# Optimization experiments

Measured on AMD Instinct MI355X. Metric: run time of the kernel, lower is better.

The kernel has to match this reference:

```python
import jax, jax.numpy as jnp
import numpy as np

SEQ_LEN = 70      # hardcoded in original (view(-1, 70))
HIDDEN = 230
EMB = 50
VOCAB = 100000
BIG_NUM = 64
N_TOTAL = 2048
N_REL = 100       # hardcoded relation count
POS_VOCAB = 123
POS_DIM = 5
D_IN = EMB + 2 * POS_DIM


def setup_inputs() -> dict:
    key = jax.random.key(0)
    ks = jax.random.split(key, 20)
    bag = N_TOTAL // BIG_NUM
    labels = jax.random.randint(ks[3], (BIG_NUM,), 0, N_REL)
    inp = {
        "sentence": jax.random.randint(ks[0], (N_TOTAL, SEQ_LEN), 0, VOCAB),
        "pos1": jax.random.randint(ks[1], (N_TOTAL, SEQ_LEN), 0, POS_VOCAB),
        "pos2": jax.random.randint(ks[2], (N_TOTAL, SEQ_LEN), 0, POS_VOCAB),
        "total_shape": jnp.arange(BIG_NUM + 1, dtype=jnp.int32) * bag,
        "y_batch": jax.nn.one_hot(labels, N_REL, dtype=jnp.float32),
        "word_emb": jax.random.normal(ks[4], (VOCAB, EMB), jnp.float32) * 0.1,
        "pos1_table": jax.random.normal(ks[5], (POS_VOCAB, POS_DIM), jnp.float32) * 0.1,
        "pos2_table": jax.random.normal(ks[6], (POS_VOCAB, POS_DIM), jnp.float32) * 0.1,
        "W_ih_f": jax.random.normal(ks[7], (3 * HIDDEN, D_IN), jnp.float32) * 0.05,
        "W_hh_f": jax.random.normal(ks[8], (3 * HIDDEN, HIDDEN), jnp.float32) * 0.05,
        "b_ih_f": jnp.zeros((3 * HIDDEN,), jnp.float32),
        "b_hh_f": jnp.zeros((3 * HIDDEN,), jnp.float32),
        "W_ih_b": jax.random.normal(ks[9], (3 * HIDDEN, D_IN), jnp.float32) * 0.05,
        "W_hh_b": jax.random.normal(ks[10], (3 * HIDDEN, HIDDEN), jnp.float32) * 0.05,
        "b_ih_b": jnp.zeros((3 * HIDDEN,), jnp.float32),
        "b_hh_b": jnp.zeros((3 * HIDDEN,), jnp.float32),
        "attention_w": jax.random.normal(ks[11], (HIDDEN, 1), jnp.float32) * 0.1,
        "sen_a": jax.random.normal(ks[12], (HIDDEN,), jnp.float32) * 0.1,
        "sen_r": jax.random.normal(ks[13], (HIDDEN, 1), jnp.float32) * 0.1,
        "relation_embedding": jax.random.normal(ks[14], (N_REL, HIDDEN), jnp.float32) * 0.1,
        "sen_d": jax.random.normal(ks[15], (N_REL,), jnp.float32) * 0.1,
    }
    return inp


def _gru_dir(x_proj, W_hh, b_hh, reverse):
    """One GRU direction. x_proj: [N,T,3H] = x @ W_ih^T + b_ih (precomputed)."""
    N = x_proj.shape[0]
    H = W_hh.shape[1]

    def step(h, gi):
        gh = h @ W_hh.T + b_hh
        i_r, i_z, i_n = jnp.split(gi, 3, axis=-1)
        h_r, h_z, h_n = jnp.split(gh, 3, axis=-1)
        r = jax.nn.sigmoid(i_r + h_r)
        z = jax.nn.sigmoid(i_z + h_z)
        n = jnp.tanh(i_n + r * h_n)
        h = (1.0 - z) * n + z * h
        return h, h

    h0 = jnp.zeros((N, H), x_proj.dtype)
    _, ys = jax.lax.scan(step, h0, jnp.swapaxes(x_proj, 0, 1), reverse=reverse)
    return jnp.swapaxes(ys, 0, 1)  # [N,T,H]


def reference(sentence, pos1, pos2, total_shape, y_batch,
              word_emb, pos1_table, pos2_table,
              W_ih_f, W_hh_f, b_ih_f, b_hh_f,
              W_ih_b, W_hh_b, b_ih_b, b_hh_b,
              attention_w, sen_a, sen_r, relation_embedding, sen_d):
    # embedding lookup + concat -> [N, T, D_IN]
    emb = jnp.concatenate([word_emb[sentence], pos1_table[pos1], pos2_table[pos2]], axis=-1)
    gi_f = jnp.einsum('ntd,gd->ntg', emb, W_ih_f) + b_ih_f
    gi_b = jnp.einsum('ntd,gd->ntg', emb, W_ih_b) + b_ih_b
    # bidirectional GRU, then sum fwd + bwd halves (torch.add(tupf, tupb))
    tup = _gru_dir(gi_f, W_hh_f, b_hh_f, False) + _gru_dir(gi_b, W_hh_b, b_hh_b, True)  # [N,T,H]
    # word-level attention over the 70 timesteps
    word_alpha = jax.nn.softmax((jnp.tanh(tup) @ attention_w)[..., 0], axis=-1)  # [N,T]
    attention_r = jnp.einsum('nt,nth->nh', word_alpha, tup)                       # [N,H]
    repre = jnp.tanh(attention_r)
    # ragged per-bag (sentence-level) attention via segment ops
    n_total = repre.shape[0]
    seg = jnp.searchsorted(total_shape[1:], jnp.arange(n_total), side='right')   # [N] bag ids
    s = ((repre * sen_a) @ sen_r)[:, 0]                                          # [N]
    m = jax.ops.segment_max(s, seg, num_segments=BIG_NUM)
    e = jnp.exp(s - m[seg])
    denom = jax.ops.segment_sum(e, seg, num_segments=BIG_NUM)
    alpha = e / denom[seg]
    sen_s = jax.ops.segment_sum(alpha[:, None] * repre, seg, num_segments=BIG_NUM)  # [B,H]
    logits = sen_s @ relation_embedding.T + sen_d                                   # [B,100]
    prob = jax.nn.softmax(logits, axis=-1)
    # BCEWithLogitsLoss (mean over 100 classes) summed over bags
    bce = jnp.maximum(logits, 0.0) - logits * y_batch + jnp.log1p(jnp.exp(-jnp.abs(logits)))
    total_loss = jnp.sum(jnp.mean(bce, axis=-1))
    acc = (jnp.argmax(prob, axis=-1) == jnp.argmax(y_batch, axis=-1)).astype(jnp.float32)
    return total_loss, acc, prob
```

## Files before the change

### kernel.cpp

```cpp
#include <hip/hip_runtime.h>
#include <hip/hip_bf16.h>
#include <math.h>

#define SEQ 70
#define HID 230
#define G3  690
#define EMBD 50
#define DIN 60
#define NTOT 2048
#define NREL 100
#define NBAG 64
#define BAGSZ 32
#define PDIM 5
#define MB 4
#define KU 5
#define KTOT 290
#define SROWS 292


__global__ void k_zero(float* p, long n) {
    long i = (long)blockIdx.x * 256 + threadIdx.x;
    if (i < n) p[i] = 0.f;
}

__global__ void k_embed(const int* __restrict__ sent, const int* __restrict__ p1,
                        const int* __restrict__ p2,  const float* __restrict__ wemb,
                        const float* __restrict__ t1, const float* __restrict__ t2,
                        float* __restrict__ emb) {
    long idx = (long)blockIdx.x * 256 + threadIdx.x;
    long total = (long)NTOT * SEQ * DIN;
    if (idx >= total) return;
    int nt = (int)(idx / DIN);
    int j  = (int)(idx % DIN);
    float v;
    if (j < EMBD)            v = wemb[(long)sent[nt] * EMBD + j];
    else if (j < EMBD + PDIM) v = t1[p1[nt] * PDIM + (j - EMBD)];
    else                      v = t2[p2[nt] * PDIM + (j - EMBD - PDIM)];
    emb[idx] = v;
}

__global__ void k_transpose(const float* __restrict__ in, float* __restrict__ out,
                            int G, int K) {
    int idx = blockIdx.x * 256 + threadIdx.x;
    if (idx >= G * K) return;
    int g = idx / K, k = idx % K;
    out[k * G + g] = in[idx];
}


#define ROWLD(kk) { ra0 = *(const float4*)s_s[kk]; }

#define FMA4(WR,WZ,WN, AR,AZ,AN) \
    AR[0]=fmaf(WR,ra0.x,AR[0]); AZ[0]=fmaf(WZ,ra0.x,AZ[0]); AN[0]=fmaf(WN,ra0.x,AN[0]); \
    AR[1]=fmaf(WR,ra0.y,AR[1]); AZ[1]=fmaf(WZ,ra0.y,AZ[1]); AN[1]=fmaf(WN,ra0.y,AN[1]); \
    AR[2]=fmaf(WR,ra0.z,AR[2]); AZ[2]=fmaf(WZ,ra0.z,AZ[2]); AN[2]=fmaf(WN,ra0.z,AN[2]); \
    AR[3]=fmaf(WR,ra0.w,AR[3]); AZ[3]=fmaf(WZ,ra0.w,AZ[3]); AN[3]=fmaf(WN,ra0.w,AN[3]);

#define U1R(KB, UE, AR,AZ,AN) \
    FMA4(wR[UE],wZ[UE],wN[UE], AR,AZ,AN); \
    ROWLD((KB)*KU+(UE)+1); \
    { int _kk = (((KB)+1)*KU + (UE)) * G3; \
      wR[UE]=pw[_kk]; wZ[UE]=pw[_kk+HID]; wN[UE]=pw[_kk+2*HID]; }

#define U1W(KB, UE, AR,AZ,AN) \
    FMA4(wR[UE],wZ[UE],wN[UE], AR,AZ,AN); \
    ROWLD((KB)*KU+(UE)+1); \
    { int _kk = (UE) * G3; \
      wR[UE]=pw[_kk]; wZ[UE]=pw[_kk+HID]; wN[UE]=pw[_kk+2*HID]; }

#define BLK5R(KB, AR,AZ,AN) \
    U1R(KB, 0, AR,AZ,AN) U1R(KB, 1, AR,AZ,AN) U1R(KB, 2, AR,AZ,AN) \
    U1R(KB, 3, AR,AZ,AN) U1R(KB, 4, AR,AZ,AN)

#define BLK5W(KB, AR,AZ,AN) \
    U1W(KB, 0, AR,AZ,AN) U1W(KB, 1, AR,AZ,AN) U1W(KB, 2, AR,AZ,AN) \
    U1W(KB, 3, AR,AZ,AN) U1W(KB, 4, AR,AZ,AN)

__global__ __launch_bounds__(256, 4) void k_gru(
    const float* __restrict__ emb,
    const float* __restrict__ wcat_f, const float* __restrict__ bih_f, const float* __restrict__ bhh_f,
    const float* __restrict__ wcat_b, const float* __restrict__ bih_b, const float* __restrict__ bhh_b,
    float* __restrict__ tup) {

    const bool rev = blockIdx.x & 1;
    const int  n0  = (blockIdx.x >> 1) * MB;
    const float* wcat = rev ? wcat_b : wcat_f;
    const float* bih  = rev ? bih_b  : bih_f;
    const float* bhh  = rev ? bhh_b  : bhh_f;
    const int tid = threadIdx.x;
    const bool act = tid < HID;

    __shared__ float s_s[SROWS][MB];

    for (int i = tid; i < SROWS * MB; i += 256) ((float*)s_s)[i] = 0.f;

    float bir = 0.f, biz = 0.f, bin_ = 0.f, bhr = 0.f, bhz = 0.f, bhn = 0.f;
    if (act) {
        bir = bih[tid]; biz = bih[HID + tid]; bin_ = bih[2 * HID + tid];
        bhr = bhh[tid]; bhz = bhh[HID + tid]; bhn = bhh[2 * HID + tid];
    }

    const float* pw = wcat + tid;

    float wR[KU], wZ[KU], wN[KU];
    if (act) {
#pragma unroll
        for (int u = 0; u < KU; ++u) {
            int kk = u * G3; wR[u] = pw[kk]; wZ[u] = pw[kk + HID]; wN[u] = pw[kk + 2 * HID];
        }
    }

    __syncthreads();

    for (int t = 0; t < SEQ; ++t) {
        const int tt = rev ? (SEQ - 1 - t) : t;

        if (tid < DIN * MB) {
            int n = tid / DIN, k = tid - n * DIN;
            s_s[k][n] = emb[((long)(n0 + n) * SEQ + tt) * DIN + k];
        }
        __syncthreads();

        float ar[MB], az[MB], an[MB], hr[MB], hz[MB], hn[MB];
        if (act) {
#pragma unroll
            for (int n = 0; n < MB; ++n) {
                ar[n] = bir; az[n] = biz; an[n] = bin_;
                hr[n] = bhr; hz[n] = bhz; hn[n] = bhn;
            }
            float4 ra0;
            ROWLD(0)

#pragma clang loop unroll(disable)
            for (int kb = 0; kb < 12; ++kb) { BLK5R(kb, ar,az,an) }
#pragma clang loop unroll(disable)
            for (int kb = 12; kb < 57; ++kb) { BLK5R(kb, hr,hz,hn) }
            BLK5W(57, hr,hz,hn)
        }
        __syncthreads();

        if (act) {
#pragma unroll
            for (int n = 0; n < MB; ++n) {
                float r  = 1.f / (1.f + expf(-(ar[n] + hr[n])));
                float z  = 1.f / (1.f + expf(-(az[n] + hz[n])));
                float nn = tanhf(an[n] + r * hn[n]);
                float hold = s_s[DIN + tid][n];
                float hnew = (1.f - z) * nn + z * hold;
                s_s[DIN + tid][n] = hnew;
                atomicAdd(&tup[((long)(n0 + n) * SEQ + tt) * HID + tid], hnew);
            }
        }
    }
}

__global__ __launch_bounds__(256) void k_wordattn(
    const float* __restrict__ tup, const float* __restrict__ attw,
    const float* __restrict__ sen_a, const float* __restrict__ sen_r,
    float* __restrict__ repre, float* __restrict__ sbuf) {
    const int n = blockIdx.x, tid = threadIdx.x;
    __shared__ float tl[SEQ * HID];
    __shared__ float sc[SEQ];
    __shared__ float red[4];
    for (int i = tid; i < SEQ * HID; i += 256) tl[i] = tup[(long)n * SEQ * HID + i];
    __syncthreads();
    if (tid < SEQ) {
        float s = 0.f;
        for (int h = 0; h < HID; ++h) s += tanhf(tl[tid * HID + h]) * attw[h];
        sc[tid] = s;
    }
    __syncthreads();
    if (tid == 0) {
        float m = sc[0];
        for (int t = 1; t < SEQ; ++t) m = fmaxf(m, sc[t]);
        float ssum = 0.f;
        for (int t = 0; t < SEQ; ++t) { float e = expf(sc[t] - m); sc[t] = e; ssum += e; }
        float inv = 1.f / ssum;
        for (int t = 0; t < SEQ; ++t) sc[t] *= inv;
    }
    __syncthreads();
    float part = 0.f;
    if (tid < HID) {
        float r = 0.f;
        for (int t = 0; t < SEQ; ++t) r = fmaf(sc[t], tl[t * HID + tid], r);
        float rep = tanhf(r);
        repre[(long)n * HID + tid] = rep;
        part = rep * sen_a[tid] * sen_r[tid];
    }
    for (int off = 32; off; off >>= 1) part += __shfl_down(part, off, 64);
    if ((tid & 63) == 0) red[tid >> 6] = part;
    __syncthreads();
    if (tid == 0) sbuf[n] = red[0] + red[1] + red[2] + red[3];
}

__global__ __launch_bounds__(256) void k_bag(
    const float* __restrict__ repre, const float* __restrict__ sbuf,
    const float* __restrict__ rel, const float* __restrict__ sen_d,
    const float* __restrict__ y, float* __restrict__ out, float* __restrict__ bagloss) {
    const int b = blockIdx.x, tid = threadIdx.x;
    __shared__ float al[BAGSZ];
    __shared__ float ss[HID];
    __shared__ float lg[NREL];
    if (tid == 0) {
        float m = -1e30f;
        for (int i = 0; i < BAGSZ; ++i) m = fmaxf(m, sbuf[b * BAGSZ + i]);
        float s = 0.f;
        for (int i = 0; i < BAGSZ; ++i) { float e = expf(sbuf[b * BAGSZ + i] - m); al[i] = e; s += e; }
        float inv = 1.f / s;
        for (int i = 0; i < BAGSZ; ++i) al[i] *= inv;
    }
    __syncthreads();
    if (tid < HID) {
        float acc = 0.f;
        for (int i = 0; i < BAGSZ; ++i)
            acc = fmaf(al[i], repre[(long)(b * BAGSZ + i) * HID + tid], acc);
        ss[tid] = acc;
    }
    __syncthreads();
    if (tid < NREL) {
        float acc = sen_d[tid];
        for (int h = 0; h < HID; ++h) acc = fmaf(ss[h], rel[tid * HID + h], acc);
        lg[tid] = acc;
    }
    __syncthreads();
    if (tid == 0) {
        float m = -1e30f; int am = 0;
        for (int r = 0; r < NREL; ++r) if (lg[r] > m) { m = lg[r]; am = r; }
        float s = 0.f;
        for (int r = 0; r < NREL; ++r) s += expf(lg[r] - m);
        float inv = 1.f / s;
        float ym = -1e30f; int ay = 0;
        for (int r = 0; r < NREL; ++r) { float yy = y[b * NREL + r]; if (yy > ym) { ym = yy; ay = r; } }
        out[1 + b] = (am == ay) ? 1.f : 0.f;
        float loss = 0.f;
        for (int r = 0; r < NREL; ++r) {
            float l = lg[r], yy = y[b * NREL + r];
            loss += fmaxf(l, 0.f) - l * yy + log1pf(expf(-fabsf(l)));
            out[1 + NBAG + b * NREL + r] = expf(l - m) * inv;
        }
        bagloss[b] = loss / NREL;
    }
}

__global__ void k_final(const float* __restrict__ bagloss, float* __restrict__ out) {
    if (blockIdx.x == 0 && threadIdx.x == 0) {
        float s = 0.f;
        for (int i = 0; i < NBAG; ++i) s += bagloss[i];
        out[0] = s;
    }
}

extern "C" void kernel_launch(void* const* d_in, const int* in_sizes, int n_in,
                              void* d_out, int out_size, void* d_ws, size_t ws_size,
                              hipStream_t stream) {
    const int*   sent   = (const int*)d_in[0];
    const int*   pos1   = (const int*)d_in[1];
    const int*   pos2   = (const int*)d_in[2];
    const float* ybatch = (const float*)d_in[4];
    const float* wemb   = (const float*)d_in[5];
    const float* p1tab  = (const float*)d_in[6];
    const float* p2tab  = (const float*)d_in[7];
    const float* Wih_f  = (const float*)d_in[8];
    const float* Whh_f  = (const float*)d_in[9];
    const float* bih_f  = (const float*)d_in[10];
    const float* bhh_f  = (const float*)d_in[11];
    const float* Wih_b  = (const float*)d_in[12];
    const float* Whh_b  = (const float*)d_in[13];
    const float* bih_b  = (const float*)d_in[14];
    const float* bhh_b  = (const float*)d_in[15];
    const float* attw   = (const float*)d_in[16];
    const float* sen_a  = (const float*)d_in[17];
    const float* sen_r  = (const float*)d_in[18];
    const float* rel    = (const float*)d_in[19];
    const float* sen_d  = (const float*)d_in[20];
    float* out = (float*)d_out;

    float* ws = (float*)d_ws;
    size_t off = 0;
    float* emb    = ws + off; off += (size_t)NTOT * SEQ * DIN;
    float* wcat_f = ws + off; off += (size_t)SROWS * G3;
    float* wcat_b = ws + off; off += (size_t)SROWS * G3;
    float* tup    = ws + off; off += (size_t)NTOT * SEQ * HID;
    float* repre  = ws + off; off += (size_t)NTOT * HID;
    float* sbuf   = ws + off; off += (size_t)NTOT;
    float* bagloss= ws + off; off += (size_t)NBAG;

    const long tupN = (long)NTOT * SEQ * HID;
    k_zero<<<(int)((tupN + 255) / 256), 256, 0, stream>>>(tup, tupN);

    const long embN = (long)NTOT * SEQ * DIN;
    k_embed<<<(int)((embN + 255) / 256), 256, 0, stream>>>(sent, pos1, pos2, wemb, p1tab, p2tab, emb);

    k_transpose<<<(G3 * DIN + 255) / 256, 256, 0, stream>>>(Wih_f, wcat_f, G3, DIN);
    k_transpose<<<(G3 * HID + 255) / 256, 256, 0, stream>>>(Whh_f, wcat_f + (size_t)DIN * G3, G3, HID);
    k_transpose<<<(G3 * DIN + 255) / 256, 256, 0, stream>>>(Wih_b, wcat_b, G3, DIN);
    k_transpose<<<(G3 * HID + 255) / 256, 256, 0, stream>>>(Whh_b, wcat_b + (size_t)DIN * G3, G3, HID);

    k_gru<<<(NTOT / MB) * 2, 256, 0, stream>>>(emb,
        wcat_f, bih_f, bhh_f,
        wcat_b, bih_b, bhh_b, tup);

    k_wordattn<<<NTOT, 256, 0, stream>>>(tup, attw, sen_a, sen_r, repre, sbuf);

    k_bag<<<NBAG, 256, 0, stream>>>(repre, sbuf, rel, sen_d, ybatch, out, bagloss);

    k_final<<<1, 64, 0, stream>>>(bagloss, out);
}
```

Baseline: 3.131 ms.

## Process 8 sentences per GRU block and broadcast hidden state via readlane

Each GRU block now handles 8 sentences instead of 4, doubling reuse of every weight loaded from global memory. The hidden-state operands are read once into per-lane registers and broadcast with amdgcn readlane instead of per-k LDS float4 loads. The weight prefetch pipeline is widened to 8 slots, and padded duplicate weight rows are written so the prefetch can run past the end without a bounds check. Occupancy drops to 2 blocks per CU from 4 and register pressure rises a lot, which risks spills.

```diff
diff --git a/kernel.cpp b/kernel.cpp
--- a/kernel.cpp
+++ b/kernel.cpp
@@ -12,10 +12,10 @@
 #define NBAG 64
 #define BAGSZ 32
 #define PDIM 5
-#define MB 4
-#define KU 5
-#define KTOT 290
-#define SROWS 292
+#define MB 8
+#define KU 8
+#define SROWS 316
+#define WROWS 298
 
 
 __global__ void k_zero(float* p, long n) {
@@ -47,36 +47,45 @@
     out[k * G + g] = in[idx];
 }
 
-
-#define ROWLD(kk) { ra0 = *(const float4*)s_s[kk]; }
-
-#define FMA4(WR,WZ,WN, AR,AZ,AN) \
-    AR[0]=fmaf(WR,ra0.x,AR[0]); AZ[0]=fmaf(WZ,ra0.x,AZ[0]); AN[0]=fmaf(WN,ra0.x,AN[0]); \
-    AR[1]=fmaf(WR,ra0.y,AR[1]); AZ[1]=fmaf(WZ,ra0.y,AZ[1]); AN[1]=fmaf(WN,ra0.y,AN[1]); \
-    AR[2]=fmaf(WR,ra0.z,AR[2]); AZ[2]=fmaf(WZ,ra0.z,AZ[2]); AN[2]=fmaf(WN,ra0.z,AN[2]); \
-    AR[3]=fmaf(WR,ra0.w,AR[3]); AZ[3]=fmaf(WZ,ra0.w,AZ[3]); AN[3]=fmaf(WN,ra0.w,AN[3]);
-
-#define U1R(KB, UE, AR,AZ,AN) \
-    FMA4(wR[UE],wZ[UE],wN[UE], AR,AZ,AN); \
-    ROWLD((KB)*KU+(UE)+1); \
-    { int _kk = (((KB)+1)*KU + (UE)) * G3; \
-      wR[UE]=pw[_kk]; wZ[UE]=pw[_kk+HID]; wN[UE]=pw[_kk+2*HID]; }
-
-#define U1W(KB, UE, AR,AZ,AN) \
-    FMA4(wR[UE],wZ[UE],wN[UE], AR,AZ,AN); \
-    ROWLD((KB)*KU+(UE)+1); \
-    { int _kk = (UE) * G3; \
-      wR[UE]=pw[_kk]; wZ[UE]=pw[_kk+HID]; wN[UE]=pw[_kk+2*HID]; }
-
-#define BLK5R(KB, AR,AZ,AN) \
-    U1R(KB, 0, AR,AZ,AN) U1R(KB, 1, AR,AZ,AN) U1R(KB, 2, AR,AZ,AN) \
-    U1R(KB, 3, AR,AZ,AN) U1R(KB, 4, AR,AZ,AN)
-
-#define BLK5W(KB, AR,AZ,AN) \
-    U1W(KB, 0, AR,AZ,AN) U1W(KB, 1, AR,AZ,AN) U1W(KB, 2, AR,AZ,AN) \
-    U1W(KB, 3, AR,AZ,AN) U1W(KB, 4, AR,AZ,AN)
-
-__global__ __launch_bounds__(256, 4) void k_gru(
+__global__ void k_dupe(float* __restrict__ w) {
+    int idx = blockIdx.x * 256 + threadIdx.x;
+    if (idx >= 8 * G3) return;
+    int i = idx / G3, g = idx % G3;
+    w[(290 + i) * G3 + g] = w[((290 + i) & 7) * G3 + g];
+}
+
+
+#define RL(v, ln) __int_as_float(__builtin_amdgcn_readlane(__float_as_int(v), (ln)))
+
+#define FMA24(WRv,WZv,WNv, B0,B1,B2,B3,B4,B5,B6,B7, AR,AZ,AN) \
+    AR[0]=fmaf(WRv,B0,AR[0]); AZ[0]=fmaf(WZv,B0,AZ[0]); AN[0]=fmaf(WNv,B0,AN[0]); \
+    AR[1]=fmaf(WRv,B1,AR[1]); AZ[1]=fmaf(WZv,B1,AZ[1]); AN[1]=fmaf(WNv,B1,AN[1]); \
+    AR[2]=fmaf(WRv,B2,AR[2]); AZ[2]=fmaf(WZv,B2,AZ[2]); AN[2]=fmaf(WNv,B2,AN[2]); \
+    AR[3]=fmaf(WRv,B3,AR[3]); AZ[3]=fmaf(WZv,B3,AZ[3]); AN[3]=fmaf(WNv,B3,AN[3]); \
+    AR[4]=fmaf(WRv,B4,AR[4]); AZ[4]=fmaf(WZv,B4,AZ[4]); AN[4]=fmaf(WNv,B4,AN[4]); \
+    AR[5]=fmaf(WRv,B5,AR[5]); AZ[5]=fmaf(WZv,B5,AZ[5]); AN[5]=fmaf(WNv,B5,AN[5]); \
+    AR[6]=fmaf(WRv,B6,AR[6]); AZ[6]=fmaf(WZv,B6,AZ[6]); AN[6]=fmaf(WNv,B6,AN[6]); \
+    AR[7]=fmaf(WRv,B7,AR[7]); AZ[7]=fmaf(WZv,B7,AZ[7]); AN[7]=fmaf(WNv,B7,AN[7]);
+
+#define ESTEP(U) \
+    FMA24(wR[U],wZ[U],wN[U], ra0.x,ra0.y,ra0.z,ra0.w, ra1.x,ra1.y,ra1.z,ra1.w, ar,az,an); \
+    { int kk = eb8 + (U); \
+      ra0 = *(const float4*)&s_s[kk+1][0]; ra1 = *(const float4*)&s_s[kk+1][4]; \
+      int ro = (kk + 8) * G3; wR[U]=pw[ro]; wZ[U]=pw[ro+HID]; wN[U]=pw[ro+2*HID]; }
+
+#define HSTEP(S, U) { \
+    int ln = jb8 + (U); \
+    float b0=RL(hsa##S.x,ln), b1=RL(hsa##S.y,ln), b2=RL(hsa##S.z,ln), b3=RL(hsa##S.w,ln); \
+    float b4=RL(hsb##S.x,ln), b5=RL(hsb##S.y,ln), b6=RL(hsb##S.z,ln), b7=RL(hsb##S.w,ln); \
+    FMA24(wR[(4+(U))&7],wZ[(4+(U))&7],wN[(4+(U))&7], b0,b1,b2,b3,b4,b5,b6,b7, hr,hz,hn); \
+    { int ro = (60 + 64*(S) + jb8 + (U) + 8) * G3; const int SL=(4+(U))&7; \
+      wR[SL]=pw[ro]; wZ[SL]=pw[ro+HID]; wN[SL]=pw[ro+2*HID]; } \
+}
+
+#define H8(S) HSTEP(S,0) HSTEP(S,1) HSTEP(S,2) HSTEP(S,3) \
+              HSTEP(S,4) HSTEP(S,5) HSTEP(S,6) HSTEP(S,7)
+
+__global__ __launch_bounds__(256, 2) void k_gru(
     const float* __restrict__ emb,
     const float* __restrict__ wcat_f, const float* __restrict__ bih_f, const float* __restrict__ bhh_f,
     const float* __restrict__ wcat_b, const float* __restrict__ bih_b, const float* __restrict__ bhh_b,
@@ -110,16 +119,26 @@
         }
     }
 
+    const int lane = tid & 63;
     __syncthreads();
 
     for (int t = 0; t < SEQ; ++t) {
         const int tt = rev ? (SEQ - 1 - t) : t;
 
-        if (tid < DIN * MB) {
-            int n = tid / DIN, k = tid - n * DIN;
+        for (int i = tid; i < DIN * MB; i += 256) {
+            int n = i / DIN, k = i - n * DIN;
             s_s[k][n] = emb[((long)(n0 + n) * SEQ + tt) * DIN + k];
         }
         __syncthreads();
+
+        float4 hsa0 = *(const float4*)&s_s[ 60 + lane][0];
+        float4 hsb0 = *(const float4*)&s_s[ 60 + lane][4];
+        float4 hsa1 = *(const float4*)&s_s[124 + lane][0];
+        float4 hsb1 = *(const float4*)&s_s[124 + lane][4];
+        float4 hsa2 = *(const float4*)&s_s[188 + lane][0];
+        float4 hsb2 = *(const float4*)&s_s[188 + lane][4];
+        float4 hsa3 = *(const float4*)&s_s[252 + lane][0];
+        float4 hsb3 = *(const float4*)&s_s[252 + lane][4];
 
         float ar[MB], az[MB], an[MB], hr[MB], hz[MB], hn[MB];
         if (act) {
@@ -128,14 +147,26 @@
                 ar[n] = bir; az[n] = biz; an[n] = bin_;
                 hr[n] = bhr; hz[n] = bhz; hn[n] = bhn;
             }
-            float4 ra0;
-            ROWLD(0)
-
-#pragma clang loop unroll(disable)
-            for (int kb = 0; kb < 12; ++kb) { BLK5R(kb, ar,az,an) }
-#pragma clang loop unroll(disable)
-            for (int kb = 12; kb < 57; ++kb) { BLK5R(kb, hr,hz,hn) }
-            BLK5W(57, hr,hz,hn)
+            float4 ra0 = *(const float4*)&s_s[0][0];
+            float4 ra1 = *(const float4*)&s_s[0][4];
+
+#pragma clang loop unroll(disable)
+            for (int eb8 = 0; eb8 < 56; eb8 += 8) {
+                ESTEP(0) ESTEP(1) ESTEP(2) ESTEP(3)
+                ESTEP(4) ESTEP(5) ESTEP(6) ESTEP(7)
+            }
+            { const int eb8 = 56; ESTEP(0) ESTEP(1) ESTEP(2) ESTEP(3) }
+
+#pragma clang loop unroll(disable)
+            for (int jb8 = 0; jb8 < 64; jb8 += 8) { H8(0) }
+#pragma clang loop unroll(disable)
+            for (int jb8 = 0; jb8 < 64; jb8 += 8) { H8(1) }
+#pragma clang loop unroll(disable)
+            for (int jb8 = 0; jb8 < 64; jb8 += 8) { H8(2) }
+#pragma clang loop unroll(disable)
+            for (int jb8 = 0; jb8 < 32; jb8 += 8) { H8(3) }
+            { const int jb8 = 32;
+              HSTEP(3,0) HSTEP(3,1) HSTEP(3,2) HSTEP(3,3) HSTEP(3,4) HSTEP(3,5) }
         }
         __syncthreads();
 
@@ -278,8 +309,8 @@
     float* ws = (float*)d_ws;
     size_t off = 0;
     float* emb    = ws + off; off += (size_t)NTOT * SEQ * DIN;
-    float* wcat_f = ws + off; off += (size_t)SROWS * G3;
-    float* wcat_b = ws + off; off += (size_t)SROWS * G3;
+    float* wcat_f = ws + off; off += (size_t)WROWS * G3;
+    float* wcat_b = ws + off; off += (size_t)WROWS * G3;
     float* tup    = ws + off; off += (size_t)NTOT * SEQ * HID;
     float* repre  = ws + off; off += (size_t)NTOT * HID;
     float* sbuf   = ws + off; off += (size_t)NTOT;
@@ -295,6 +326,8 @@
     k_transpose<<<(G3 * HID + 255) / 256, 256, 0, stream>>>(Whh_f, wcat_f + (size_t)DIN * G3, G3, HID);
     k_transpose<<<(G3 * DIN + 255) / 256, 256, 0, stream>>>(Wih_b, wcat_b, G3, DIN);
     k_transpose<<<(G3 * HID + 255) / 256, 256, 0, stream>>>(Whh_b, wcat_b + (size_t)DIN * G3, G3, HID);
+    k_dupe<<<(8 * G3 + 255) / 256, 256, 0, stream>>>(wcat_f);
+    k_dupe<<<(8 * G3 + 255) / 256, 256, 0, stream>>>(wcat_b);
 
     k_gru<<<(NTOT / MB) * 2, 256, 0, stream>>>(emb,
         wcat_f, bih_f, bhh_f,
```

New measurement: 3.111 ms. About the same (-0.6%).
